# Optimization experiments

Hardware: AMD Instinct MI355X
Metric: run time of the kernel (lower is better)

## Reference

```python
import jax, jax.numpy as jnp
import numpy as np

N, B, FIN, E, EDIM, H, C = 20000, 2, 256, 320000, 64, 8, 32


def setup_inputs() -> dict:
    key = jax.random.key(0)
    ks = jax.random.split(key, 12)
    s = 1.0 / np.sqrt(FIN)
    se = 1.0 / np.sqrt(EDIM)
    return {
        "x": jax.random.normal(ks[0], (N, B, FIN), jnp.float32),
        "edata": jax.random.normal(ks[1], (E, EDIM), jnp.float32),
        "edge_src": jax.random.randint(ks[2], (E,), 0, N, jnp.int32),
        "edge_dst": jax.random.randint(ks[3], (E,), 0, N, jnp.int32),
        "Wq": jax.random.normal(ks[4], (FIN, H * C), jnp.float32) * s,
        "bq": jnp.zeros((H * C,), jnp.float32),
        "Wk": jax.random.normal(ks[5], (FIN, H * C), jnp.float32) * s,
        "bk": jnp.zeros((H * C,), jnp.float32),
        "Wv": jax.random.normal(ks[6], (FIN, H * C), jnp.float32) * s,
        "bv": jnp.zeros((H * C,), jnp.float32),
        "We": jax.random.normal(ks[7], (EDIM, H * C), jnp.float32) * se,
        "Wr": jax.random.normal(ks[8], (FIN, H * C), jnp.float32) * s,
        "br": jnp.zeros((H * C,), jnp.float32),
    }


def reference(x, edata, edge_src, edge_dst, Wq, bq, Wk, bk, Wv, bv, We, Wr, br):
    # x: [N, B, FIN]; edata: [E, EDIM]
    q = (x @ Wq + bq).reshape(N, B, H, C)   # dst queries
    k = (x @ Wk + bk).reshape(N, B, H, C)   # src keys
    v = (x @ Wv + bv).reshape(N, B, H, C)   # src values
    e = (edata @ We).reshape(E, 1, H, C)    # edge feats, broadcast over batch

    scale = 1.0 / np.sqrt(C)
    # per-edge logits: (u_mul_v / sqrt(C) + edata).sum(-1) -> [E, B, H]
    logits = (k[edge_src] * q[edge_dst] * scale + e).sum(-1)

    # edge_softmax over edges sharing the same destination node
    m = jax.ops.segment_max(logits, edge_dst, num_segments=N)      # [N, B, H]
    ex = jnp.exp(logits - m[edge_dst])
    z = jax.ops.segment_sum(ex, edge_dst, num_segments=N)          # [N, B, H]
    alpha = ex / z[edge_dst]                                       # [E, B, H]

    # weighted scatter-sum aggregation: u_mul_e + sum over dst
    att_v = v[edge_src] * alpha[..., None]                         # [E, B, H, C]
    agg = jax.ops.segment_sum(att_v, edge_dst, num_segments=N)     # [N, B, H, C]

    out = agg.reshape(N, B, H * C) + (x @ Wr + br)
    return out
```

## Files before the change

### kernel.cpp

```cpp
#include <hip/hip_runtime.h>
#include <hip/hip_bf16.h>

#define NN    20000
#define BB    2
#define EE    320000
#define MROWS (NN * BB)

typedef __bf16 bf16x8 __attribute__((ext_vector_type(8)));
typedef __bf16 bf16x4 __attribute__((ext_vector_type(4)));
typedef float  floatx4 __attribute__((ext_vector_type(4)));


#define NB_HIST 1250
#define NB_CVT  1250

__global__ __launch_bounds__(256) void prep_kernel(
    const float* __restrict__ Wq, const float* __restrict__ Wk,
    const float* __restrict__ Wv, const float* __restrict__ Wr,
    __hip_bfloat16* __restrict__ wt,
    const float* __restrict__ bq, const float* __restrict__ bk,
    const float* __restrict__ bv, const float* __restrict__ br,
    float* __restrict__ bcat,
    const float* __restrict__ We, float* __restrict__ wesum,
    const int* __restrict__ edst, int* __restrict__ counts,
    const float* __restrict__ x, __bf16* __restrict__ xb) {
  __shared__ float TA[32][65];
  __shared__ float TB[32][65];
  int bt = blockIdx.x;
  int t = threadIdx.x;

  if (bt < 16) {
    const float *A, *B;
    int c0, jbase;
    if (bt < 8) { A = Wk; B = Wv; c0 = 32 * bt;      jbase = 64 * bt; }
    else        { A = Wq; B = Wr; c0 = 32 * (bt-8);  jbase = 512 + 64 * (bt-8); }
    int krow = t >> 2;
    int cc = (t & 3) * 8;
    int sel = t >> 7;
    int u = t & 127;
    int ci = u >> 2;
    int kk0 = (u & 3) * 16;

    for (int kt = 0; kt < 4; ++kt) {
      int k = kt * 64 + krow;
      float4 a0 = *(const float4*)(A + (size_t)k * 256 + c0 + cc);
      float4 a1 = *(const float4*)(A + (size_t)k * 256 + c0 + cc + 4);
      float4 b0 = *(const float4*)(B + (size_t)k * 256 + c0 + cc);
      float4 b1 = *(const float4*)(B + (size_t)k * 256 + c0 + cc + 4);
      __syncthreads();
      TA[cc+0][krow]=a0.x; TA[cc+1][krow]=a0.y; TA[cc+2][krow]=a0.z; TA[cc+3][krow]=a0.w;
      TA[cc+4][krow]=a1.x; TA[cc+5][krow]=a1.y; TA[cc+6][krow]=a1.z; TA[cc+7][krow]=a1.w;
      TB[cc+0][krow]=b0.x; TB[cc+1][krow]=b0.y; TB[cc+2][krow]=b0.z; TB[cc+3][krow]=b0.w;
      TB[cc+4][krow]=b1.x; TB[cc+5][krow]=b1.y; TB[cc+6][krow]=b1.z; TB[cc+7][krow]=b1.w;
      __syncthreads();
      float (*T)[65] = sel ? TB : TA;
      int j = jbase + 2 * ci + sel;
      __hip_bfloat16* dst = wt + (size_t)j * 256 + kt * 64 + kk0;
      #pragma unroll
      for (int q = 0; q < 16; ++q) dst[q] = __float2bfloat16(T[ci][kk0 + q]);
    }
  } else if (bt == 16) {
    #pragma unroll
    for (int jj = 0; jj < 4; ++jj) {
      int j = jj * 256 + t;
      float val;
      if (j < 512) { int c = j >> 1;         val = (j & 1) ? bv[c] : bk[c]; }
      else         { int c = (j - 512) >> 1; val = (j & 1) ? br[c] : bq[c]; }
      bcat[j] = val;
    }
    #pragma unroll
    for (int ii = 0; ii < 2; ++ii) {
      int i = ii * 256 + t;
      int h = i >> 6, d = i & 63;
      float s = 0.f;
      for (int c = 0; c < 32; ++c) s += We[(size_t)d * 256 + h * 32 + c];
      wesum[h * 64 + d] = s;
    }
  } else if (bt < 17 + NB_HIST) {
    int e = (bt - 17) * 256 + t;
    if (e < EE) atomicAdd(&counts[edst[e]], 1);
  } else {
    int cb = bt - 17 - NB_HIST;
    size_t base = (size_t)cb * 8192 + t * 4;
    #pragma unroll
    for (int j = 0; j < 8; ++j) {
      float4 v = *(const float4*)(x + base + j * 1024);
      bf16x4 o;
      o[0] = (__bf16)v.x; o[1] = (__bf16)v.y;
      o[2] = (__bf16)v.z; o[3] = (__bf16)v.w;
      *(bf16x4*)(xb + base + j * 1024) = o;
    }
  }
}

#define SCAN_PAD (79 * 256)
__global__ __launch_bounds__(256) void scan_kernel(
    const int* __restrict__ counts,
    int* __restrict__ offsets,
    int* __restrict__ cursor) {
  __shared__ int lc[SCAN_PAD];
  __shared__ int part[256];
  int t = threadIdx.x;
  for (int j = 0; j < 79; ++j) {
    int idx = j * 256 + t;
    lc[idx] = (idx < NN) ? counts[idx] : 0;
  }
  __syncthreads();
  int lo = t * 79;
  int s = 0;
  #pragma unroll 4
  for (int i = 0; i < 79; ++i) s += lc[lo + i];
  part[t] = s;
  __syncthreads();
  for (int off = 1; off < 256; off <<= 1) {
    int v = (t >= off) ? part[t - off] : 0;
    __syncthreads();
    part[t] += v;
    __syncthreads();
  }
  int base = (t == 0) ? 0 : part[t - 1];
  for (int i = 0; i < 79; ++i) {
    int c = lc[lo + i];
    lc[lo + i] = base;
    base += c;
  }
  if (t == 255) offsets[NN] = base;
  __syncthreads();
  for (int j = 0; j < 79; ++j) {
    int idx = j * 256 + t;
    if (idx < NN) {
      int v = lc[idx];
      offsets[idx] = v;
      cursor[idx]  = v;
    }
  }
}

__global__ __launch_bounds__(256) void scatter_esum(
    const int* __restrict__ edst, const int* __restrict__ esrc,
    int* __restrict__ cursor,
    const float* __restrict__ edata, const float* __restrict__ wesum,
    int* __restrict__ ssrc, float* __restrict__ esum) {
  __shared__ float wl[512];
  int t = threadIdx.x;
  wl[t] = wesum[t];
  wl[t + 256] = wesum[t + 256];
  __syncthreads();
  int e = blockIdx.x * 256 + t;
  int p = atomicAdd(&cursor[edst[e]], 1);
  ssrc[p] = esrc[e];
  float acc[8] = {};
  const float* row = edata + (size_t)e * 64;
  for (int d = 0; d < 64; d += 4) {
    float4 v = *(const float4*)(row + d);
    #pragma unroll
    for (int hh = 0; hh < 8; ++hh) {
      const float* wv = &wl[hh * 64 + d];
      acc[hh] += v.x * wv[0] + v.y * wv[1] + v.z * wv[2] + v.w * wv[3];
    }
  }
  float* op = esum + (size_t)p * 8;
  *(float4*)op       = make_float4(acc[0], acc[1], acc[2], acc[3]);
  *(float4*)(op + 4) = make_float4(acc[4], acc[5], acc[6], acc[7]);
}

__global__ __launch_bounds__(256) void gemm_qkvr(
    const __bf16* __restrict__ xb,
    const __bf16* __restrict__ wt,
    const float* __restrict__ bcat,
    __hip_bfloat16* __restrict__ out) {
  const int LSTR = 72;
  __shared__ __attribute__((aligned(16))) __bf16 As[64 * LSTR];

  int m0 = blockIdx.y * 64;
  int n0 = blockIdx.x * 256;
  int t = threadIdx.x;
  int w = t >> 6, l = t & 63;
  int lr = l & 15, lq = l >> 4;
  int ar = t >> 2, ac = (t & 3) * 16;

  floatx4 acc[4][4] = {};
  const __bf16* wbase = wt + (size_t)(n0 + 64 * w + lr) * 256 + lq * 8;

  for (int ks = 0; ks < 4; ++ks) {
    const __bf16* xp = xb + (size_t)(m0 + ar) * 256 + ks * 64 + ac;
    bf16x8 a0 = *(const bf16x8*)xp;
    bf16x8 a1 = *(const bf16x8*)(xp + 8);
    bf16x8 bfr[2][4];
    #pragma unroll
    for (int kk = 0; kk < 2; ++kk)
      #pragma unroll
      for (int nt = 0; nt < 4; ++nt)
        bfr[kk][nt] = *(const bf16x8*)(wbase + (size_t)nt * 16 * 256 + ks * 64 + kk * 32);
    __syncthreads();
    *(bf16x8*)&As[ar * LSTR + ac]     = a0;
    *(bf16x8*)&As[ar * LSTR + ac + 8] = a1;
    __syncthreads();
    #pragma unroll
    for (int kk = 0; kk < 2; ++kk) {
      bf16x8 af[4];
      #pragma unroll
      for (int mt = 0; mt < 4; ++mt)
        af[mt] = *(const bf16x8*)&As[(16 * mt + lr) * LSTR + kk * 32 + lq * 8];
      #pragma unroll
      for (int mt = 0; mt < 4; ++mt)
        #pragma unroll
        for (int nt = 0; nt < 4; ++nt)
          acc[mt][nt] = __builtin_amdgcn_mfma_f32_16x16x32_bf16(af[mt], bfr[kk][nt], acc[mt][nt], 0, 0, 0);
    }
  }

  #pragma unroll
  for (int mt = 0; mt < 4; ++mt)
    #pragma unroll
    for (int nt = 0; nt < 4; ++nt)
      #pragma unroll
      for (int r = 0; r < 4; ++r) {
        int gr = m0 + 16 * mt + lq * 4 + r;
        int gc = n0 + 64 * w + 16 * nt + lr;
        out[(size_t)gr * 1024 + gc] = __float2bfloat16(acc[mt][nt][r] + bcat[gc]);
      }
}

#define LOADSLOT(KV, EV, IDX)                                        \
  { int s_ = __builtin_amdgcn_readlane(s_l, (IDX));                  \
    KV = *(const uint4*)(kvl + (size_t)s_ * 1024);                   \
    EV = esp[(size_t)(IDX) * 8]; }

#define CONSUME(KV, EV)                                              \
  { float part = __uint_as_float(KV.x << 16) * q0                    \
               + __uint_as_float(KV.y << 16) * q1                    \
               + __uint_as_float(KV.z << 16) * q2                    \
               + __uint_as_float(KV.w << 16) * q3;                   \
    part += __shfl_xor(part, 1, 64);                                 \
    part += __shfl_xor(part, 2, 64);                                 \
    part += __shfl_xor(part, 4, 64);                                 \
    float p = __expf(part * 0.17677669529663687f + EV);              \
    z += p;                                                          \
    a0 += p * __uint_as_float(KV.x & 0xFFFF0000u);                   \
    a1 += p * __uint_as_float(KV.y & 0xFFFF0000u);                   \
    a2 += p * __uint_as_float(KV.z & 0xFFFF0000u);                   \
    a3 += p * __uint_as_float(KV.w & 0xFFFF0000u); }

__global__ __launch_bounds__(256) void aggregate_kernel(
    const unsigned int* __restrict__ qkvr,
    const float* __restrict__ esum,
    const int* __restrict__ offsets,
    const int* __restrict__ ssrc,
    float* __restrict__ out) {
  int t = threadIdx.x;
  int w = t >> 6, l = t & 63;
  int nb = blockIdx.x * 4 + w;
  int b = nb & 1, n = nb >> 1;
  int h = l >> 3;
  int beg = offsets[n], end = offsets[n + 1];

  uint4 qr4 = *(const uint4*)(qkvr + (size_t)nb * 512 + 256 + l * 4);
  float q0 = __uint_as_float(qr4.x << 16), q1 = __uint_as_float(qr4.y << 16);
  float q2 = __uint_as_float(qr4.z << 16), q3 = __uint_as_float(qr4.w << 16);

  const unsigned* kvl = qkvr + (size_t)b * 512 + l * 4;

  float z = 0.f, a0 = 0.f, a1 = 0.f, a2 = 0.f, a3 = 0.f;

  for (int base = beg; base < end; base += 64) {
    int chunk = min(64, end - base);
    int s_l = (l < chunk) ? ssrc[base + l] : 0;
    const float* esp = esum + (size_t)base * 8 + h;
    uint4 k0 = {0,0,0,0}, k1 = {0,0,0,0}, k2 = {0,0,0,0};
    uint4 k3 = {0,0,0,0}, k4 = {0,0,0,0}, k5 = {0,0,0,0};
    float e0 = 0.f, e1 = 0.f, e2 = 0.f, e3 = 0.f, e4 = 0.f, e5 = 0.f;
    LOADSLOT(k0, e0, 0);
    if (chunk > 1) LOADSLOT(k1, e1, 1);
    if (chunk > 2) LOADSLOT(k2, e2, 2);
    if (chunk > 3) LOADSLOT(k3, e3, 3);
    if (chunk > 4) LOADSLOT(k4, e4, 4);
    if (chunk > 5) LOADSLOT(k5, e5, 5);
    for (int i = 0; i < chunk; i += 6) {
      CONSUME(k0, e0);
      if (i + 6 < chunk) LOADSLOT(k0, e0, i + 6);
      if (i + 1 < chunk) {
        CONSUME(k1, e1);
        if (i + 7 < chunk) LOADSLOT(k1, e1, i + 7);
        if (i + 2 < chunk) {
          CONSUME(k2, e2);
          if (i + 8 < chunk) LOADSLOT(k2, e2, i + 8);
          if (i + 3 < chunk) {
            CONSUME(k3, e3);
            if (i + 9 < chunk) LOADSLOT(k3, e3, i + 9);
            if (i + 4 < chunk) {
              CONSUME(k4, e4);
              if (i + 10 < chunk) LOADSLOT(k4, e4, i + 10);
              if (i + 5 < chunk) {
                CONSUME(k5, e5);
                if (i + 11 < chunk) LOADSLOT(k5, e5, i + 11);
              }
            }
          }
        }
      }
    }
  }
  float inv = (z > 0.f) ? (1.0f / z) : 0.f;
  float4 o = make_float4(a0 * inv + __uint_as_float(qr4.x & 0xFFFF0000u),
                         a1 * inv + __uint_as_float(qr4.y & 0xFFFF0000u),
                         a2 * inv + __uint_as_float(qr4.z & 0xFFFF0000u),
                         a3 * inv + __uint_as_float(qr4.w & 0xFFFF0000u));
  *(float4*)(out + (size_t)nb * 256 + l * 4) = o;
}

extern "C" void kernel_launch(void* const* d_in, const int* in_sizes, int n_in,
                              void* d_out, int out_size, void* d_ws, size_t ws_size,
                              hipStream_t stream) {
  (void)in_sizes; (void)n_in; (void)out_size; (void)ws_size;
  const float* x     = (const float*)d_in[0];
  const float* edata = (const float*)d_in[1];
  const int* esrc    = (const int*)d_in[2];
  const int* edst    = (const int*)d_in[3];
  const float* Wq    = (const float*)d_in[4];
  const float* bq    = (const float*)d_in[5];
  const float* Wk    = (const float*)d_in[6];
  const float* bk    = (const float*)d_in[7];
  const float* Wv    = (const float*)d_in[8];
  const float* bv    = (const float*)d_in[9];
  const float* We    = (const float*)d_in[10];
  const float* Wr    = (const float*)d_in[11];
  const float* br    = (const float*)d_in[12];
  float* out = (float*)d_out;

  char* ws = (char*)d_ws;
  size_t off = 0;
  auto carve = [&](size_t bytes) -> void* {
    void* p = ws + off;
    off += (bytes + 255) & ~(size_t)255;
    return p;
  };
  int* counts    = (int*)carve((size_t)NN * 4);
  int* offsets   = (int*)carve((size_t)(NN + 1) * 4);
  int* cursor    = (int*)carve((size_t)NN * 4);
  int* ssrc      = (int*)carve((size_t)EE * 4);
  __hip_bfloat16* wt = (__hip_bfloat16*)carve((size_t)1024 * 256 * 2);
  float* bcat    = (float*)carve(1024 * 4);
  float* wesum   = (float*)carve(8 * 64 * 4);
  float* esum    = (float*)carve((size_t)EE * 8 * 4);
  __bf16* xb     = (__bf16*)carve((size_t)MROWS * 256 * 2);
  __hip_bfloat16* qkvr = (__hip_bfloat16*)carve((size_t)MROWS * 1024 * 2);

  hipMemsetAsync(counts, 0, (size_t)NN * 4, stream);
  prep_kernel<<<17 + NB_HIST + NB_CVT, 256, 0, stream>>>(
      Wq, Wk, Wv, Wr, wt, bq, bk, bv, br, bcat, We, wesum, edst, counts, x, xb);
  scan_kernel<<<1, 256, 0, stream>>>(counts, offsets, cursor);
  scatter_esum<<<EE / 256, 256, 0, stream>>>(edst, esrc, cursor, edata, wesum,
                                             ssrc, esum);
  gemm_qkvr<<<dim3(4, 625), 256, 0, stream>>>(xb, (const __bf16*)wt, bcat, qkvr);
  aggregate_kernel<<<MROWS / 4, 256, 0, stream>>>((const unsigned int*)qkvr, esum,
                                                  offsets, ssrc, out);
}
```

Before: 382.1 us.

## Fuse fp32-to-bf16 conversion into GEMM and degree-sort nodes for aggregation

Drops the separate x-to-bf16 conversion pass and its workspace buffer. The GEMM now loads fp32 x directly, converts it once into a full-K LDS tile, and loops over all four 256-column output slices per block, so A is reused across N. The scan kernel also builds a degree-bucketed permutation of nodes, and the aggregation kernel processes nodes in that order so waves with similar edge counts run together, reducing load imbalance. The costs are a larger LDS footprint per GEMM block, fewer GEMM blocks, an extra indirection, and less locality in the output writes.

```diff
diff --git a/kernel.cpp b/kernel.cpp
--- a/kernel.cpp
+++ b/kernel.cpp
@@ -12,7 +12,6 @@
 
 
 #define NB_HIST 1250
-#define NB_CVT  1250
 
 __global__ __launch_bounds__(256) void prep_kernel(
     const float* __restrict__ Wq, const float* __restrict__ Wk,
@@ -22,8 +21,7 @@
     const float* __restrict__ bv, const float* __restrict__ br,
     float* __restrict__ bcat,
     const float* __restrict__ We, float* __restrict__ wesum,
-    const int* __restrict__ edst, int* __restrict__ counts,
-    const float* __restrict__ x, __bf16* __restrict__ xb) {
+    const int* __restrict__ edst, int* __restrict__ counts) {
   __shared__ float TA[32][65];
   __shared__ float TB[32][65];
   int bt = blockIdx.x;
@@ -76,20 +74,9 @@
       for (int c = 0; c < 32; ++c) s += We[(size_t)d * 256 + h * 32 + c];
       wesum[h * 64 + d] = s;
     }
-  } else if (bt < 17 + NB_HIST) {
+  } else {
     int e = (bt - 17) * 256 + t;
     if (e < EE) atomicAdd(&counts[edst[e]], 1);
-  } else {
-    int cb = bt - 17 - NB_HIST;
-    size_t base = (size_t)cb * 8192 + t * 4;
-    #pragma unroll
-    for (int j = 0; j < 8; ++j) {
-      float4 v = *(const float4*)(x + base + j * 1024);
-      bf16x4 o;
-      o[0] = (__bf16)v.x; o[1] = (__bf16)v.y;
-      o[2] = (__bf16)v.z; o[3] = (__bf16)v.w;
-      *(bf16x4*)(xb + base + j * 1024) = o;
-    }
   }
 }
 
@@ -97,13 +84,19 @@
 __global__ __launch_bounds__(256) void scan_kernel(
     const int* __restrict__ counts,
     int* __restrict__ offsets,
-    int* __restrict__ cursor) {
+    int* __restrict__ cursor,
+    int* __restrict__ perm) {
   __shared__ int lc[SCAN_PAD];
   __shared__ int part[256];
-  int t = threadIdx.x;
+  __shared__ int dh[64];
+  int t = threadIdx.x;
+  if (t < 64) dh[t] = 0;
+  __syncthreads();
   for (int j = 0; j < 79; ++j) {
     int idx = j * 256 + t;
-    lc[idx] = (idx < NN) ? counts[idx] : 0;
+    int c = (idx < NN) ? counts[idx] : 0;
+    lc[idx] = c;
+    if (idx < NN) atomicAdd(&dh[c < 63 ? c : 63], 1);
   }
   __syncthreads();
   int lo = t * 79;
@@ -117,6 +110,10 @@
     __syncthreads();
     part[t] += v;
     __syncthreads();
+  }
+  if (t == 0) {
+    int b = 0;
+    for (int i = 0; i < 64; ++i) { int c = dh[i]; dh[i] = b; b += c; }
   }
   int base = (t == 0) ? 0 : part[t - 1];
   for (int i = 0; i < 79; ++i) {
@@ -132,6 +129,9 @@
       int v = lc[idx];
       offsets[idx] = v;
       cursor[idx]  = v;
+      int c = counts[idx];
+      int pos = atomicAdd(&dh[c < 63 ? c : 63], 1);
+      perm[pos] = idx;
     }
   }
 }
@@ -165,61 +165,70 @@
 }
 
 __global__ __launch_bounds__(256) void gemm_qkvr(
-    const __bf16* __restrict__ xb,
+    const float* __restrict__ x,
     const __bf16* __restrict__ wt,
     const float* __restrict__ bcat,
     __hip_bfloat16* __restrict__ out) {
-  const int LSTR = 72;
+  const int LSTR = 264;
   __shared__ __attribute__((aligned(16))) __bf16 As[64 * LSTR];
 
-  int m0 = blockIdx.y * 64;
-  int n0 = blockIdx.x * 256;
+  int m0 = blockIdx.x * 64;
   int t = threadIdx.x;
   int w = t >> 6, l = t & 63;
   int lr = l & 15, lq = l >> 4;
-  int ar = t >> 2, ac = (t & 3) * 16;
-
-  floatx4 acc[4][4] = {};
-  const __bf16* wbase = wt + (size_t)(n0 + 64 * w + lr) * 256 + lq * 8;
-
-  for (int ks = 0; ks < 4; ++ks) {
-    const __bf16* xp = xb + (size_t)(m0 + ar) * 256 + ks * 64 + ac;
-    bf16x8 a0 = *(const bf16x8*)xp;
-    bf16x8 a1 = *(const bf16x8*)(xp + 8);
-    bf16x8 bfr[2][4];
-    #pragma unroll
-    for (int kk = 0; kk < 2; ++kk)
+  int ar = t >> 2, c0 = (t & 3) * 8;
+
+  const float* xp = x + (size_t)(m0 + ar) * 256 + c0;
+  #pragma unroll
+  for (int j = 0; j < 8; ++j) {
+    float4 f0 = *(const float4*)(xp + j * 32);
+    float4 f1 = *(const float4*)(xp + j * 32 + 4);
+    bf16x8 av;
+    av[0] = (__bf16)f0.x; av[1] = (__bf16)f0.y;
+    av[2] = (__bf16)f0.z; av[3] = (__bf16)f0.w;
+    av[4] = (__bf16)f1.x; av[5] = (__bf16)f1.y;
+    av[6] = (__bf16)f1.z; av[7] = (__bf16)f1.w;
+    *(bf16x8*)&As[ar * LSTR + c0 + j * 32] = av;
+  }
+  __syncthreads();
+
+  #pragma unroll 1
+  for (int p = 0; p < 4; ++p) {
+    int n0 = p * 256;
+    floatx4 acc[4][4] = {};
+    const __bf16* wbase = wt + (size_t)(n0 + 64 * w + lr) * 256 + lq * 8;
+    #pragma unroll
+    for (int ks = 0; ks < 4; ++ks) {
+      bf16x8 bfr[2][4];
+      #pragma unroll
+      for (int kk = 0; kk < 2; ++kk)
+        #pragma unroll
+        for (int nt = 0; nt < 4; ++nt)
+          bfr[kk][nt] = *(const bf16x8*)(wbase + (size_t)nt * 16 * 256 + ks * 64 + kk * 32);
+      #pragma unroll
+      for (int kk = 0; kk < 2; ++kk) {
+        bf16x8 af[4];
+        #pragma unroll
+        for (int mt = 0; mt < 4; ++mt)
+          af[mt] = *(const bf16x8*)&As[(16 * mt + lr) * LSTR + ks * 64 + kk * 32 + lq * 8];
+        #pragma unroll
+        for (int mt = 0; mt < 4; ++mt)
+          #pragma unroll
+          for (int nt = 0; nt < 4; ++nt)
+            acc[mt][nt] = __builtin_amdgcn_mfma_f32_16x16x32_bf16(af[mt], bfr[kk][nt], acc[mt][nt], 0, 0, 0);
+      }
+    }
+    #pragma unroll
+    for (int mt = 0; mt < 4; ++mt)
       #pragma unroll
       for (int nt = 0; nt < 4; ++nt)
-        bfr[kk][nt] = *(const bf16x8*)(wbase + (size_t)nt * 16 * 256 + ks * 64 + kk * 32);
-    __syncthreads();
-    *(bf16x8*)&As[ar * LSTR + ac]     = a0;
-    *(bf16x8*)&As[ar * LSTR + ac + 8] = a1;
-    __syncthreads();
-    #pragma unroll
-    for (int kk = 0; kk < 2; ++kk) {
-      bf16x8 af[4];
-      #pragma unroll
-      for (int mt = 0; mt < 4; ++mt)
-        af[mt] = *(const bf16x8*)&As[(16 * mt + lr) * LSTR + kk * 32 + lq * 8];
-      #pragma unroll
-      for (int mt = 0; mt < 4; ++mt)
         #pragma unroll
-        for (int nt = 0; nt < 4; ++nt)
-          acc[mt][nt] = __builtin_amdgcn_mfma_f32_16x16x32_bf16(af[mt], bfr[kk][nt], acc[mt][nt], 0, 0, 0);
-    }
-  }
-
-  #pragma unroll
-  for (int mt = 0; mt < 4; ++mt)
-    #pragma unroll
-    for (int nt = 0; nt < 4; ++nt)
-      #pragma unroll
-      for (int r = 0; r < 4; ++r) {
-        int gr = m0 + 16 * mt + lq * 4 + r;
-        int gc = n0 + 64 * w + 16 * nt + lr;
-        out[(size_t)gr * 1024 + gc] = __float2bfloat16(acc[mt][nt][r] + bcat[gc]);
-      }
+        for (int r = 0; r < 4; ++r) {
+          int gr = m0 + 16 * mt + lq * 4 + r;
+          int gc = n0 + 64 * w + 16 * nt + lr;
+          out[(size_t)gr * 1024 + gc] = __float2bfloat16(acc[mt][nt][r] + bcat[gc]);
+        }
+  }
 }
 
 #define LOADSLOT(KV, EV, IDX)                                        \
@@ -247,11 +256,14 @@
     const float* __restrict__ esum,
     const int* __restrict__ offsets,
     const int* __restrict__ ssrc,
+    const int* __restrict__ perm,
     float* __restrict__ out) {
   int t = threadIdx.x;
   int w = t >> 6, l = t & 63;
-  int nb = blockIdx.x * 4 + w;
-  int b = nb & 1, n = nb >> 1;
+  int idx = blockIdx.x * 4 + w;
+  int n = perm[idx >> 1];
+  int b = idx & 1;
+  int nb = 2 * n + b;
   int h = l >> 3;
   int beg = offsets[n], end = offsets[n + 1];
 
@@ -338,21 +350,21 @@
   int* counts    = (int*)carve((size_t)NN * 4);
   int* offsets   = (int*)carve((size_t)(NN + 1) * 4);
   int* cursor    = (int*)carve((size_t)NN * 4);
+  int* perm      = (int*)carve((size_t)NN * 4);
   int* ssrc      = (int*)carve((size_t)EE * 4);
   __hip_bfloat16* wt = (__hip_bfloat16*)carve((size_t)1024 * 256 * 2);
   float* bcat    = (float*)carve(1024 * 4);
   float* wesum   = (float*)carve(8 * 64 * 4);
   float* esum    = (float*)carve((size_t)EE * 8 * 4);
-  __bf16* xb     = (__bf16*)carve((size_t)MROWS * 256 * 2);
   __hip_bfloat16* qkvr = (__hip_bfloat16*)carve((size_t)MROWS * 1024 * 2);
 
   hipMemsetAsync(counts, 0, (size_t)NN * 4, stream);
-  prep_kernel<<<17 + NB_HIST + NB_CVT, 256, 0, stream>>>(
-      Wq, Wk, Wv, Wr, wt, bq, bk, bv, br, bcat, We, wesum, edst, counts, x, xb);
-  scan_kernel<<<1, 256, 0, stream>>>(counts, offsets, cursor);
+  prep_kernel<<<17 + NB_HIST, 256, 0, stream>>>(
+      Wq, Wk, Wv, Wr, wt, bq, bk, bv, br, bcat, We, wesum, edst, counts);
+  scan_kernel<<<1, 256, 0, stream>>>(counts, offsets, cursor, perm);
   scatter_esum<<<EE / 256, 256, 0, stream>>>(edst, esrc, cursor, edata, wesum,
                                              ssrc, esum);
-  gemm_qkvr<<<dim3(4, 625), 256, 0, stream>>>(xb, (const __bf16*)wt, bcat, qkvr);
+  gemm_qkvr<<<MROWS / 64, 256, 0, stream>>>(x, (const __bf16*)wt, bcat, qkvr);
   aggregate_kernel<<<MROWS / 4, 256, 0, stream>>>((const unsigned int*)qkvr, esum,
-                                                  offsets, ssrc, out);
-}
+                                                  offsets, ssrc, perm, out);
+}
```

Result: slower. 438.3 us (+14.7%).

## Load GEMM A fragments directly from global and swizzle block order

Applied to the files above, without the earlier changes.

The QKVR GEMM stops staging the x tile through shared memory. Each wave now loads its A fragments straight from global into registers, which removes both __syncthreads per k-step. The launch becomes a 1D grid remapped so that groups of 8 row tiles share all four column tiles, which should improve L2 reuse of x. The cost is that every wave reloads the full 64-row A tile from global/L2 (4x redundant reads across waves) and uses more registers.

```diff
diff --git a/kernel.cpp b/kernel.cpp
--- a/kernel.cpp
+++ b/kernel.cpp
@@ -169,45 +169,41 @@
     const __bf16* __restrict__ wt,
     const float* __restrict__ bcat,
     __hip_bfloat16* __restrict__ out) {
-  const int LSTR = 72;
-  __shared__ __attribute__((aligned(16))) __bf16 As[64 * LSTR];
-
-  int m0 = blockIdx.y * 64;
-  int n0 = blockIdx.x * 256;
+  int bid = blockIdx.x;
+  int g, p;
+  if (bid >= 2496) { g = 624; p = bid - 2496; }
+  else { g = ((bid >> 5) << 3) | (bid & 7); p = (bid >> 3) & 3; }
+  int m0 = g * 64;
+  int n0 = p * 256;
   int t = threadIdx.x;
   int w = t >> 6, l = t & 63;
   int lr = l & 15, lq = l >> 4;
-  int ar = t >> 2, ac = (t & 3) * 16;
+
+  const __bf16* abase = xb + (size_t)(m0 + lr) * 256 + lq * 8;
+  const __bf16* wbase = wt + (size_t)(n0 + 64 * w + lr) * 256 + lq * 8;
 
   floatx4 acc[4][4] = {};
-  const __bf16* wbase = wt + (size_t)(n0 + 64 * w + lr) * 256 + lq * 8;
-
+
+  #pragma unroll
   for (int ks = 0; ks < 4; ++ks) {
-    const __bf16* xp = xb + (size_t)(m0 + ar) * 256 + ks * 64 + ac;
-    bf16x8 a0 = *(const bf16x8*)xp;
-    bf16x8 a1 = *(const bf16x8*)(xp + 8);
-    bf16x8 bfr[2][4];
+    bf16x8 af[2][4], bfr[2][4];
+    #pragma unroll
+    for (int kk = 0; kk < 2; ++kk)
+      #pragma unroll
+      for (int mt = 0; mt < 4; ++mt)
+        af[kk][mt] = *(const bf16x8*)(abase + (size_t)mt * 16 * 256 + ks * 64 + kk * 32);
     #pragma unroll
     for (int kk = 0; kk < 2; ++kk)
       #pragma unroll
       for (int nt = 0; nt < 4; ++nt)
         bfr[kk][nt] = *(const bf16x8*)(wbase + (size_t)nt * 16 * 256 + ks * 64 + kk * 32);
-    __syncthreads();
-    *(bf16x8*)&As[ar * LSTR + ac]     = a0;
-    *(bf16x8*)&As[ar * LSTR + ac + 8] = a1;
-    __syncthreads();
-    #pragma unroll
-    for (int kk = 0; kk < 2; ++kk) {
-      bf16x8 af[4];
-      #pragma unroll
-      for (int mt = 0; mt < 4; ++mt)
-        af[mt] = *(const bf16x8*)&As[(16 * mt + lr) * LSTR + kk * 32 + lq * 8];
+    #pragma unroll
+    for (int kk = 0; kk < 2; ++kk)
       #pragma unroll
       for (int mt = 0; mt < 4; ++mt)
         #pragma unroll
         for (int nt = 0; nt < 4; ++nt)
-          acc[mt][nt] = __builtin_amdgcn_mfma_f32_16x16x32_bf16(af[mt], bfr[kk][nt], acc[mt][nt], 0, 0, 0);
-    }
+          acc[mt][nt] = __builtin_amdgcn_mfma_f32_16x16x32_bf16(af[kk][mt], bfr[kk][nt], acc[mt][nt], 0, 0, 0);
   }
 
   #pragma unroll
@@ -216,7 +212,7 @@
     for (int nt = 0; nt < 4; ++nt)
       #pragma unroll
       for (int r = 0; r < 4; ++r) {
-        int gr = m0 + 16 * mt + lq * 4 + r;
+        int gr = m0 + 16 * mt + (l >> 4) * 4 + r;
         int gc = n0 + 64 * w + 16 * nt + lr;
         out[(size_t)gr * 1024 + gc] = __float2bfloat16(acc[mt][nt][r] + bcat[gc]);
       }
@@ -352,7 +348,7 @@
   scan_kernel<<<1, 256, 0, stream>>>(counts, offsets, cursor);
   scatter_esum<<<EE / 256, 256, 0, stream>>>(edst, esrc, cursor, edata, wesum,
                                              ssrc, esum);
-  gemm_qkvr<<<dim3(4, 625), 256, 0, stream>>>(xb, (const __bf16*)wt, bcat, qkvr);
+  gemm_qkvr<<<2500, 256, 0, stream>>>(xb, (const __bf16*)wt, bcat, qkvr);
   aggregate_kernel<<<MROWS / 4, 256, 0, stream>>>((const unsigned int*)qkvr, esum,
                                                   offsets, ssrc, out);
 }
```

New measurement: 410.8 us. 7.5% more time.

## Split each wave into two half-waves processing alternate edges with 8 channels per lane

Applied to the files above, without the earlier changes.

The aggregate kernel now has each 32-lane half of a wave handle a different edge, with every lane covering 8 channels instead of 4. The per-edge dot-product reduction uses DPP quad shuffles instead of three xor shuffles. The two halves' softmax sums and accumulators are merged with a cross-half shuffle at the end. This doubles the edges in flight per wave and shortens the reduction chain, at the cost of more registers per lane, a final cross-half reduction, and half the lanes idling in the tail when a chunk has few edges.

```diff
diff --git a/kernel.cpp b/kernel.cpp
--- a/kernel.cpp
+++ b/kernel.cpp
@@ -222,25 +222,43 @@
       }
 }
 
-#define LOADSLOT(KV, EV, IDX)                                        \
-  { int s_ = __builtin_amdgcn_readlane(s_l, (IDX));                  \
-    KV = *(const uint4*)(kvl + (size_t)s_ * 1024);                   \
-    EV = esp[(size_t)(IDX) * 8]; }
-
-#define CONSUME(KV, EV)                                              \
-  { float part = __uint_as_float(KV.x << 16) * q0                    \
-               + __uint_as_float(KV.y << 16) * q1                    \
-               + __uint_as_float(KV.z << 16) * q2                    \
-               + __uint_as_float(KV.w << 16) * q3;                   \
-    part += __shfl_xor(part, 1, 64);                                 \
-    part += __shfl_xor(part, 2, 64);                                 \
-    part += __shfl_xor(part, 4, 64);                                 \
-    float p = __expf(part * 0.17677669529663687f + EV);              \
-    z += p;                                                          \
-    a0 += p * __uint_as_float(KV.x & 0xFFFF0000u);                   \
-    a1 += p * __uint_as_float(KV.y & 0xFFFF0000u);                   \
-    a2 += p * __uint_as_float(KV.z & 0xFFFF0000u);                   \
-    a3 += p * __uint_as_float(KV.w & 0xFFFF0000u); }
+__device__ __forceinline__ float quad_reduce(float x) {
+  x += __int_as_float(__builtin_amdgcn_update_dpp(
+      0, __float_as_int(x), 0xB1, 0xF, 0xF, true));
+  x += __int_as_float(__builtin_amdgcn_update_dpp(
+      0, __float_as_int(x), 0x4E, 0xF, 0xF, true));
+  return x;
+}
+
+#define LOADSLOT(KA, KB, EV, IT)                                       \
+  { int sa_ = __builtin_amdgcn_readlane(s_l, (IT));                    \
+    int sb_ = __builtin_amdgcn_readlane(s_l, (IT) + 32);               \
+    if ((IT) < cnt) {                                                  \
+      const unsigned* p_ = kvl + (size_t)(half ? sb_ : sa_) * 1024;    \
+      KA = *(const uint4*)p_;                                          \
+      KB = *(const uint4*)(p_ + 4);                                    \
+      EV = esp[(size_t)(IT) * 8];                                      \
+    } }
+
+#define RELOAD(KA, KB, EV, IT) { EV = -INFINITY; LOADSLOT(KA, KB, EV, IT) }
+
+#define CONSUME(KA, KB, EV)                                            \
+  { float part =                                                       \
+      __uint_as_float(KA.x << 16) * q0 + __uint_as_float(KA.y << 16) * q1  \
+    + __uint_as_float(KA.z << 16) * q2 + __uint_as_float(KA.w << 16) * q3  \
+    + __uint_as_float(KB.x << 16) * q4 + __uint_as_float(KB.y << 16) * q5  \
+    + __uint_as_float(KB.z << 16) * q6 + __uint_as_float(KB.w << 16) * q7; \
+    part = quad_reduce(part);                                          \
+    float p = __expf(part * 0.17677669529663687f + EV);                \
+    z += p;                                                            \
+    a0 += p * __uint_as_float(KA.x & 0xFFFF0000u);                     \
+    a1 += p * __uint_as_float(KA.y & 0xFFFF0000u);                     \
+    a2 += p * __uint_as_float(KA.z & 0xFFFF0000u);                     \
+    a3 += p * __uint_as_float(KA.w & 0xFFFF0000u);                     \
+    a4 += p * __uint_as_float(KB.x & 0xFFFF0000u);                     \
+    a5 += p * __uint_as_float(KB.y & 0xFFFF0000u);                     \
+    a6 += p * __uint_as_float(KB.z & 0xFFFF0000u);                     \
+    a7 += p * __uint_as_float(KB.w & 0xFFFF0000u); }
 
 __global__ __launch_bounds__(256) void aggregate_kernel(
     const unsigned int* __restrict__ qkvr,
@@ -252,61 +270,78 @@
   int w = t >> 6, l = t & 63;
   int nb = blockIdx.x * 4 + w;
   int b = nb & 1, n = nb >> 1;
-  int h = l >> 3;
+  int half = l >> 5, u = l & 31;
+  int h = u >> 2;
+  int coff = h * 32 + (u & 3) * 8;
   int beg = offsets[n], end = offsets[n + 1];
 
-  uint4 qr4 = *(const uint4*)(qkvr + (size_t)nb * 512 + 256 + l * 4);
-  float q0 = __uint_as_float(qr4.x << 16), q1 = __uint_as_float(qr4.y << 16);
-  float q2 = __uint_as_float(qr4.z << 16), q3 = __uint_as_float(qr4.w << 16);
-
-  const unsigned* kvl = qkvr + (size_t)b * 512 + l * 4;
-
-  float z = 0.f, a0 = 0.f, a1 = 0.f, a2 = 0.f, a3 = 0.f;
+  const unsigned* qrp = qkvr + (size_t)nb * 512 + 256 + coff;
+  uint4 qa = *(const uint4*)qrp;
+  uint4 qb = *(const uint4*)(qrp + 4);
+  float q0 = __uint_as_float(qa.x << 16), q1 = __uint_as_float(qa.y << 16);
+  float q2 = __uint_as_float(qa.z << 16), q3 = __uint_as_float(qa.w << 16);
+  float q4 = __uint_as_float(qb.x << 16), q5 = __uint_as_float(qb.y << 16);
+  float q6 = __uint_as_float(qb.z << 16), q7 = __uint_as_float(qb.w << 16);
+
+  const unsigned* kvl = qkvr + (size_t)b * 512 + coff;
+
+  float z = 0.f;
+  float a0 = 0.f, a1 = 0.f, a2 = 0.f, a3 = 0.f;
+  float a4 = 0.f, a5 = 0.f, a6 = 0.f, a7 = 0.f;
 
   for (int base = beg; base < end; base += 64) {
     int chunk = min(64, end - base);
     int s_l = (l < chunk) ? ssrc[base + l] : 0;
-    const float* esp = esum + (size_t)base * 8 + h;
-    uint4 k0 = {0,0,0,0}, k1 = {0,0,0,0}, k2 = {0,0,0,0};
-    uint4 k3 = {0,0,0,0}, k4 = {0,0,0,0}, k5 = {0,0,0,0};
-    float e0 = 0.f, e1 = 0.f, e2 = 0.f, e3 = 0.f, e4 = 0.f, e5 = 0.f;
-    LOADSLOT(k0, e0, 0);
-    if (chunk > 1) LOADSLOT(k1, e1, 1);
-    if (chunk > 2) LOADSLOT(k2, e2, 2);
-    if (chunk > 3) LOADSLOT(k3, e3, 3);
-    if (chunk > 4) LOADSLOT(k4, e4, 4);
-    if (chunk > 5) LOADSLOT(k5, e5, 5);
-    for (int i = 0; i < chunk; i += 6) {
-      CONSUME(k0, e0);
-      if (i + 6 < chunk) LOADSLOT(k0, e0, i + 6);
-      if (i + 1 < chunk) {
-        CONSUME(k1, e1);
-        if (i + 7 < chunk) LOADSLOT(k1, e1, i + 7);
-        if (i + 2 < chunk) {
-          CONSUME(k2, e2);
-          if (i + 8 < chunk) LOADSLOT(k2, e2, i + 8);
-          if (i + 3 < chunk) {
-            CONSUME(k3, e3);
-            if (i + 9 < chunk) LOADSLOT(k3, e3, i + 9);
-            if (i + 4 < chunk) {
-              CONSUME(k4, e4);
-              if (i + 10 < chunk) LOADSLOT(k4, e4, i + 10);
-              if (i + 5 < chunk) {
-                CONSUME(k5, e5);
-                if (i + 11 < chunk) LOADSLOT(k5, e5, i + 11);
-              }
-            }
+    int itmax = chunk < 32 ? chunk : 32;
+    int cnt = half ? chunk - 32 : itmax;
+    const float* esp = esum + ((size_t)base + (half ? 32 : 0)) * 8 + h;
+    uint4 k0a = {0,0,0,0}, k0b = {0,0,0,0}, k1a = {0,0,0,0}, k1b = {0,0,0,0};
+    uint4 k2a = {0,0,0,0}, k2b = {0,0,0,0}, k3a = {0,0,0,0}, k3b = {0,0,0,0};
+    float e0 = -INFINITY, e1 = -INFINITY, e2 = -INFINITY, e3 = -INFINITY;
+    LOADSLOT(k0a, k0b, e0, 0)
+    LOADSLOT(k1a, k1b, e1, 1)
+    LOADSLOT(k2a, k2b, e2, 2)
+    LOADSLOT(k3a, k3b, e3, 3)
+    for (int i = 0; i < itmax; i += 4) {
+      CONSUME(k0a, k0b, e0)
+      if (i + 4 < itmax) RELOAD(k0a, k0b, e0, i + 4)
+      if (i + 1 < itmax) {
+        CONSUME(k1a, k1b, e1)
+        if (i + 5 < itmax) RELOAD(k1a, k1b, e1, i + 5)
+        if (i + 2 < itmax) {
+          CONSUME(k2a, k2b, e2)
+          if (i + 6 < itmax) RELOAD(k2a, k2b, e2, i + 6)
+          if (i + 3 < itmax) {
+            CONSUME(k3a, k3b, e3)
+            if (i + 7 < itmax) RELOAD(k3a, k3b, e3, i + 7)
           }
         }
       }
     }
   }
-  float inv = (z > 0.f) ? (1.0f / z) : 0.f;
-  float4 o = make_float4(a0 * inv + __uint_as_float(qr4.x & 0xFFFF0000u),
-                         a1 * inv + __uint_as_float(qr4.y & 0xFFFF0000u),
-                         a2 * inv + __uint_as_float(qr4.z & 0xFFFF0000u),
-                         a3 * inv + __uint_as_float(qr4.w & 0xFFFF0000u));
-  *(float4*)(out + (size_t)nb * 256 + l * 4) = o;
+
+  z  += __shfl_xor(z, 32, 64);
+  a0 += __shfl_xor(a0, 32, 64);  a1 += __shfl_xor(a1, 32, 64);
+  a2 += __shfl_xor(a2, 32, 64);  a3 += __shfl_xor(a3, 32, 64);
+  a4 += __shfl_xor(a4, 32, 64);  a5 += __shfl_xor(a5, 32, 64);
+  a6 += __shfl_xor(a6, 32, 64);  a7 += __shfl_xor(a7, 32, 64);
+
+  if (half == 0) {
+    float inv = (z > 0.f) ? (1.0f / z) : 0.f;
+    float r0 = __uint_as_float(qa.x & 0xFFFF0000u);
+    float r1 = __uint_as_float(qa.y & 0xFFFF0000u);
+    float r2 = __uint_as_float(qa.z & 0xFFFF0000u);
+    float r3 = __uint_as_float(qa.w & 0xFFFF0000u);
+    float r4 = __uint_as_float(qb.x & 0xFFFF0000u);
+    float r5 = __uint_as_float(qb.y & 0xFFFF0000u);
+    float r6 = __uint_as_float(qb.z & 0xFFFF0000u);
+    float r7 = __uint_as_float(qb.w & 0xFFFF0000u);
+    float* op = out + (size_t)nb * 256 + coff;
+    *(float4*)op       = make_float4(a0 * inv + r0, a1 * inv + r1,
+                                     a2 * inv + r2, a3 * inv + r3);
+    *(float4*)(op + 4) = make_float4(a4 * inv + r4, a5 * inv + r5,
+                                     a6 * inv + r6, a7 * inv + r7);
+  }
 }
 
 extern "C" void kernel_launch(void* const* d_in, const int* in_sizes, int n_in,
```

After: 376.5 us. No clear change (-1.5%).
